# Kernel tuning notes

Measured on AMD Instinct MI355X. Metric: run time of the kernel, lower is better.

Reference implementation:

```python
import jax, jax.numpy as jnp
import numpy as np

N_NODES = 50000
N_EDGES = 1250000
IN_CH = 64
HID = 64
N_CLASSES = 10
N_GRAPHS = 128


def _xavier(key, shape):
    fan_out, fan_in = shape
    limit = np.sqrt(6.0 / (fan_in + fan_out))
    return jax.random.uniform(key, shape, jnp.float32, -limit, limit)


def setup_inputs() -> dict:
    key = jax.random.key(0)
    ks = jax.random.split(key, 12)
    x = jax.random.normal(ks[0], (N_NODES, IN_CH), jnp.float32)
    edge_index = jax.random.randint(ks[1], (2, N_EDGES), 0, N_NODES, jnp.int64)
    batch = jnp.sort(jax.random.randint(ks[2], (N_NODES,), 0, N_GRAPHS, jnp.int64))
    return {
        "x": x,
        "edge_index": edge_index,
        "batch": batch,
        # GraphConv i: lin_rel (weight+bias) applied to aggregated neighbors,
        # lin_root (no bias) applied to self features. Weights are [out, in].
        "W1_rel": _xavier(ks[3], (HID, IN_CH)), "b1": jnp.zeros((HID,), jnp.float32),
        "W1_root": _xavier(ks[4], (HID, IN_CH)),
        "W2_rel": _xavier(ks[5], (HID, HID)), "b2": jnp.zeros((HID,), jnp.float32),
        "W2_root": _xavier(ks[6], (HID, HID)),
        "W3_rel": _xavier(ks[7], (HID, HID)), "b3": jnp.zeros((HID,), jnp.float32),
        "W3_root": _xavier(ks[8], (HID, HID)),
        "W_lin": _xavier(ks[9], (N_CLASSES, HID)), "b_lin": jnp.zeros((N_CLASSES,), jnp.float32),
    }


def _graph_conv(x, src, dst, W_rel, b, W_root):
    # sum-aggregate neighbor features: gather at src, scatter-add at dst
    agg = jax.ops.segment_sum(x[src], dst, num_segments=N_NODES)  # [N, F]
    return agg @ W_rel.T + b + x @ W_root.T


def reference(x, edge_index, batch, W1_rel, b1, W1_root, W2_rel, b2, W2_root,
              W3_rel, b3, W3_root, W_lin, b_lin):
    src, dst = edge_index[0], edge_index[1]
    h = jax.nn.relu(_graph_conv(x, src, dst, W1_rel, b1, W1_root))
    h = jax.nn.relu(_graph_conv(h, src, dst, W2_rel, b2, W2_root))
    h = _graph_conv(h, src, dst, W3_rel, b3, W3_root)
    # global mean pool over graphs
    sums = jax.ops.segment_sum(h, batch, num_segments=N_GRAPHS)        # [G, HID]
    counts = jax.ops.segment_sum(jnp.ones((h.shape[0],), h.dtype), batch,
                                 num_segments=N_GRAPHS)
    pooled = sums / jnp.maximum(counts, 1.0)[:, None]
    out = pooled @ W_lin.T + b_lin  # dropout inactive in eval mode
    return (pooled, out)
```

## Files before the change

### kernel.cpp

```cpp
#include <hip/hip_runtime.h>

#define N_NODES   50000
#define HID       64
#define N_GRAPHS  128
#define N_CLASSES 10
#define NP        196
#define EPA       8192
#define PCAP      8192

typedef __attribute__((ext_vector_type(8))) short short8;
typedef __attribute__((ext_vector_type(4))) float f32x4;

__device__ __forceinline__ unsigned bf16rne(float f) {
    unsigned u = __float_as_uint(f);
    return (u + 0x7fffu + ((u >> 16) & 1u)) >> 16;
}
__device__ __forceinline__ unsigned pack_bf16x2(float lo, float hi) {
    return bf16rne(lo) | (bf16rne(hi) << 16);
}


__global__ void cvt_kernel(const float* __restrict__ x, unsigned short* __restrict__ xb,
                           int* __restrict__ gcursor) {
    if (blockIdx.x == 0 && threadIdx.x < NP) gcursor[threadIdx.x] = 0;
    int i = blockIdx.x * blockDim.x + threadIdx.x;
    if (i < N_NODES * 16) {
        float4 v = ((const float4*)x)[i];
        uint2 o;
        o.x = pack_bf16x2(v.x, v.y);
        o.y = pack_bf16x2(v.z, v.w);
        ((uint2*)xb)[i] = o;
    }
}


__global__ __launch_bounds__(256) void bucket_kernel(
    const int* __restrict__ src, const int* __restrict__ dst,
    int* __restrict__ gcursor, unsigned* __restrict__ packed, int E) {
    __shared__ int hist[NP], scp[NP], base[NP], cnt2[NP];
    __shared__ int sc[256];
    __shared__ unsigned stag[EPA];
    const int t = threadIdx.x;
    const int e0 = blockIdx.x * EPA;
    const int e1 = min(e0 + EPA, E);
    for (int i = t; i < NP; i += 256) { hist[i] = 0; cnt2[i] = 0; }
    __syncthreads();
    for (int e = e0 + t; e < e1; e += 256)
        atomicAdd(&hist[dst[e] >> 8], 1);
    __syncthreads();
    sc[t] = (t < NP) ? hist[t] : 0;
    __syncthreads();
    for (int off = 1; off < 256; off <<= 1) {
        int add = (t >= off) ? sc[t - off] : 0;
        __syncthreads();
        sc[t] += add;
        __syncthreads();
    }
    if (t < NP) {
        scp[t] = sc[t] - hist[t];
        if (hist[t] > 0) base[t] = atomicAdd(&gcursor[t], hist[t]);
    }
    __syncthreads();
    for (int e = e0 + t; e < e1; e += 256) {
        int d = dst[e], s = src[e];
        int p = d >> 8;
        int idx = scp[p] + atomicAdd(&cnt2[p], 1);
        stag[idx] = (unsigned)s | ((unsigned)(d & 255) << 16) | ((unsigned)p << 24);
    }
    __syncthreads();
    const int n = e1 - e0;
    for (int i = t; i < n; i += 256) {
        unsigned v = stag[i];
        int p = v >> 24;
        packed[(size_t)p * PCAP + base[p] + (i - scp[p])] = v & 0x00FFFFFFu;
    }
}

__global__ __launch_bounds__(256) void build_kernel(
    const unsigned* __restrict__ packed, const int* __restrict__ gcursor,
    int* __restrict__ offsets, unsigned short* __restrict__ csr) {
    __shared__ int hist[256], lofs[256], cnt[256], sc[256], gv[256];
    __shared__ unsigned short lcsr[PCAP];
    const int p = blockIdx.x, t = threadIdx.x;

    int v = (t < NP) ? gcursor[t] : 0;
    sc[t] = v; gv[t] = v;
    __syncthreads();
    for (int off = 1; off < 256; off <<= 1) {
        int add = (t >= off) ? sc[t - off] : 0;
        __syncthreads();
        sc[t] += add;
        __syncthreads();
    }
    const int pb = sc[p] - gv[p];
    const int ne = gv[p];
    if (p == NP - 1 && t == 0) offsets[N_NODES] = sc[NP - 1];
    __syncthreads();

    const unsigned* mypk = packed + (size_t)p * PCAP;
    hist[t] = 0; cnt[t] = 0;
    __syncthreads();
    for (int i = t; i < ne; i += 256)
        atomicAdd(&hist[(mypk[i] >> 16) & 255], 1);
    __syncthreads();
    sc[t] = hist[t];
    __syncthreads();
    for (int off = 1; off < 256; off <<= 1) {
        int add = (t >= off) ? sc[t - off] : 0;
        __syncthreads();
        sc[t] += add;
        __syncthreads();
    }
    lofs[t] = sc[t] - hist[t];
    int node = p * 256 + t;
    if (node < N_NODES) offsets[node] = pb + lofs[t];
    __syncthreads();
    for (int i = t; i < ne; i += 256) {
        unsigned vv = mypk[i];
        int dl = (vv >> 16) & 255;
        int slot = lofs[dl] + atomicAdd(&cnt[dl], 1);
        lcsr[slot] = (unsigned short)(vv & 0xFFFFu);
    }
    __syncthreads();
    for (int i = t; i < ne; i += 256) csr[pb + i] = lcsr[i];
}


__global__ __launch_bounds__(256) void gather_kernel(
    const unsigned short* __restrict__ hin,
    const int* __restrict__ offsets, const unsigned short* __restrict__ csr_src,
    unsigned short* __restrict__ agg) {
    const int w = threadIdx.x >> 6, lane = threadIdx.x & 63;
    const int rg = lane >> 4, c8 = lane & 15;
    const int n = blockIdx.x * 4 + w;
    const int beg = offsets[n], end = offsets[n + 1];

    float a0 = 0.f, a1 = 0.f, a2 = 0.f, a3 = 0.f;
    for (int base = beg; base < end; base += 64) {
        int cnt = min(64, end - base);
        int sidx = (base + lane < end) ? (int)csr_src[base + lane] : 0;
        for (int kb = 0; kb < cnt; kb += 32) {
            uint2 u[8];
#pragma unroll
            for (int p = 0; p < 8; ++p) {
                int e = kb + 4 * p + rg;
                int r = __shfl(sidx, e);
                u[p] = (e < cnt) ? *(const uint2*)(hin + (size_t)r * 64 + c8 * 4)
                                 : (uint2){0u, 0u};
            }
#pragma unroll
            for (int p = 0; p < 8; ++p) {
                a0 += __uint_as_float(u[p].x << 16);
                a1 += __uint_as_float(u[p].x & 0xffff0000u);
                a2 += __uint_as_float(u[p].y << 16);
                a3 += __uint_as_float(u[p].y & 0xffff0000u);
            }
        }
    }
#pragma unroll
    for (int m = 16; m <= 32; m <<= 1) {
        a0 += __shfl_xor(a0, m);
        a1 += __shfl_xor(a1, m);
        a2 += __shfl_xor(a2, m);
        a3 += __shfl_xor(a3, m);
    }
    if (rg == 0) {
        uint2 o;
        o.x = pack_bf16x2(a0, a1);
        o.y = pack_bf16x2(a2, a3);
        *(uint2*)(agg + (size_t)n * 64 + c8 * 4) = o;
    }
}


template <int RELU>
__global__ __launch_bounds__(256) void linear_kernel(
    const unsigned short* __restrict__ agg,
    const unsigned short* __restrict__ hin,
    const float* __restrict__ Wrel, const float* __restrict__ bias,
    const float* __restrict__ Wroot, unsigned short* __restrict__ hout) {
    __shared__ unsigned short outT[4][16][72];

    const int tid = threadIdx.x;
    const int w = tid >> 6, lane = tid & 63;
    const int q = lane >> 4, c = lane & 15;
    const int g0 = (blockIdx.x * 4 + w) * 16;
    if (g0 >= N_NODES) return;

    short8 brel[4][2], broot[4][2];
    float biasv[4];
#pragma unroll
    for (int t = 0; t < 4; ++t) {
        int o = t * 16 + c;
        biasv[t] = bias[o];
#pragma unroll
        for (int s = 0; s < 2; ++s) {
            const float4* pr = (const float4*)(Wrel  + o * 64 + s * 32 + q * 8);
            const float4* po = (const float4*)(Wroot + o * 64 + s * 32 + q * 8);
            float4 r0 = pr[0], r1 = pr[1], z0 = po[0], z1 = po[1];
            short8 rr, zz;
            rr[0] = (short)bf16rne(r0.x); rr[1] = (short)bf16rne(r0.y);
            rr[2] = (short)bf16rne(r0.z); rr[3] = (short)bf16rne(r0.w);
            rr[4] = (short)bf16rne(r1.x); rr[5] = (short)bf16rne(r1.y);
            rr[6] = (short)bf16rne(r1.z); rr[7] = (short)bf16rne(r1.w);
            zz[0] = (short)bf16rne(z0.x); zz[1] = (short)bf16rne(z0.y);
            zz[2] = (short)bf16rne(z0.z); zz[3] = (short)bf16rne(z0.w);
            zz[4] = (short)bf16rne(z1.x); zz[5] = (short)bf16rne(z1.y);
            zz[6] = (short)bf16rne(z1.z); zz[7] = (short)bf16rne(z1.w);
            brel[t][s] = rr; broot[t][s] = zz;
        }
    }

    const int na = min(g0 + c, N_NODES - 1);
    short8 a_agg[2], a_x[2];
#pragma unroll
    for (int s = 0; s < 2; ++s) {
        a_agg[s] = *(const short8*)(agg + (size_t)na * 64 + s * 32 + q * 8);
        a_x[s]   = *(const short8*)(hin + (size_t)na * 64 + s * 32 + q * 8);
    }

    f32x4 acc4[4];
#pragma unroll
    for (int t = 0; t < 4; ++t) {
        f32x4 a0 = {biasv[t], biasv[t], biasv[t], biasv[t]};
        a0 = __builtin_amdgcn_mfma_f32_16x16x32_bf16(a_agg[0], brel[t][0], a0, 0, 0, 0);
        a0 = __builtin_amdgcn_mfma_f32_16x16x32_bf16(a_agg[1], brel[t][1], a0, 0, 0, 0);
        a0 = __builtin_amdgcn_mfma_f32_16x16x32_bf16(a_x[0],  broot[t][0], a0, 0, 0, 0);
        a0 = __builtin_amdgcn_mfma_f32_16x16x32_bf16(a_x[1],  broot[t][1], a0, 0, 0, 0);
        acc4[t] = a0;
    }

#pragma unroll
    for (int t = 0; t < 4; ++t)
#pragma unroll
        for (int r = 0; r < 4; ++r) {
            float v = acc4[t][r];
            if (RELU) v = fmaxf(v, 0.f);
            outT[w][q * 4 + r][t * 16 + c] = (unsigned short)bf16rne(v);
        }

#pragma unroll
    for (int it = 0; it < 2; ++it) {
        int row = it * 8 + (lane >> 3);
        int ch = (lane & 7) * 8;
        int n = g0 + row;
        if (n < N_NODES) {
            short8 v = *(const short8*)&outT[w][row][ch];
            *(short8*)(hout + (size_t)n * 64 + ch) = v;
        }
    }
}


__global__ __launch_bounds__(256) void poolfinal_kernel(
    const unsigned short* __restrict__ h, const int* __restrict__ batch,
    const float* __restrict__ Wlin, const float* __restrict__ blin,
    float* __restrict__ out) {
    __shared__ float part[4][64];
    const int g = blockIdx.x;
    const int tid = threadIdx.x, w = tid >> 6, lane = tid & 63;

    int a = 0, b = N_NODES;
    while (a < b) { int m = (a + b) >> 1; if (batch[m] < g) a = m + 1; else b = m; }
    const int lo = a;
    b = N_NODES;
    while (a < b) { int m = (a + b) >> 1; if (batch[m] < g + 1) a = m + 1; else b = m; }
    const int hi = a;

    float acc = 0.f;
    for (int n = lo + w; n < hi; n += 4) {
        unsigned u = h[(size_t)n * 64 + lane];
        acc += __uint_as_float(u << 16);
    }
    part[w][lane] = acc;
    __syncthreads();
    if (w == 0) {
        float s = part[0][lane] + part[1][lane] + part[2][lane] + part[3][lane];
        float cdiv = fmaxf((float)(hi - lo), 1.0f);
        float pv = s / cdiv;
        out[g * 64 + lane] = pv;
        part[0][lane] = pv;
    }
    __syncthreads();
    if (tid < N_CLASSES) {
        float o = blin[tid];
#pragma unroll
        for (int k = 0; k < 64; ++k) o += part[0][k] * Wlin[tid * 64 + k];
        out[N_GRAPHS * 64 + g * N_CLASSES + tid] = o;
    }
}


extern "C" void kernel_launch(void* const* d_in, const int* in_sizes, int n_in,
                              void* d_out, int out_size, void* d_ws, size_t ws_size,
                              hipStream_t stream) {
    const float* x     = (const float*)d_in[0];
    const int*   ei    = (const int*)d_in[1];
    const int*   batch = (const int*)d_in[2];
    const float* W1r = (const float*)d_in[3];
    const float* b1  = (const float*)d_in[4];
    const float* W1o = (const float*)d_in[5];
    const float* W2r = (const float*)d_in[6];
    const float* b2  = (const float*)d_in[7];
    const float* W2o = (const float*)d_in[8];
    const float* W3r = (const float*)d_in[9];
    const float* b3  = (const float*)d_in[10];
    const float* W3o = (const float*)d_in[11];
    const float* Wl  = (const float*)d_in[12];
    const float* bl  = (const float*)d_in[13];
    float* out = (float*)d_out;

    const int E = in_sizes[1] / 2;
    const int* src = ei;
    const int* dst = ei + E;

    char* p = (char*)d_ws;
    unsigned short* xb  = (unsigned short*)p; p += (size_t)N_NODES * 64 * 2;
    unsigned short* h1  = (unsigned short*)p; p += (size_t)N_NODES * 64 * 2;
    unsigned short* h2  = (unsigned short*)p; p += (size_t)N_NODES * 64 * 2;
    unsigned short* agg = (unsigned short*)p; p += (size_t)N_NODES * 64 * 2;
    unsigned short* h3  = h1;
    unsigned* packed    = (unsigned*)p; p += (size_t)NP * PCAP * 4;
    unsigned short* csr = (unsigned short*)p; p += (size_t)E * 2;
    int* offsets   = (int*)p;   p += (size_t)(N_NODES + 1) * 4;
    int* gcursor   = (int*)p;   p += NP * 4;

    const int NCHUNK = (E + EPA - 1) / EPA;
    cvt_kernel<<<(N_NODES * 16 + 255) / 256, 256, 0, stream>>>(x, xb, gcursor);
    bucket_kernel<<<NCHUNK, 256, 0, stream>>>(src, dst, gcursor, packed, E);
    build_kernel<<<NP, 256, 0, stream>>>(packed, gcursor, offsets, csr);

    const int GB = N_NODES / 4;
    const int LB = (N_NODES + 63) / 64;
    gather_kernel<<<GB, 256, 0, stream>>>(xb, offsets, csr, agg);
    linear_kernel<1><<<LB, 256, 0, stream>>>(agg, xb, W1r, b1, W1o, h1);
    gather_kernel<<<GB, 256, 0, stream>>>(h1, offsets, csr, agg);
    linear_kernel<1><<<LB, 256, 0, stream>>>(agg, h1, W2r, b2, W2o, h2);
    gather_kernel<<<GB, 256, 0, stream>>>(h2, offsets, csr, agg);
    linear_kernel<0><<<LB, 256, 0, stream>>>(agg, h2, W3r, b3, W3o, h3);

    poolfinal_kernel<<<N_GRAPHS, 256, 0, stream>>>(h3, batch, Wl, bl, out);
}
```

Baseline: 281.3 us.

## Split node feature arrays into two 32-channel slabs for cache-friendly gathers

Node features, aggregates and hidden states move from a row-major [N,64] bf16 layout to two channel slabs of [N,32] each. The gather kernel now runs twice as many blocks, each summing one slab, so the working set touched at any moment is half as large and more likely to stay in L2/MALL during the random neighbor gathers. The linear, conversion and pooling kernels are updated to read and write the slab layout. The cost is that the CSR index list and offsets are read twice per layer and each gathered row segment is only 64 bytes.

```diff
diff --git a/kernel.cpp b/kernel.cpp
--- a/kernel.cpp
+++ b/kernel.cpp
@@ -7,6 +7,8 @@
 #define NP        196
 #define EPA       8192
 #define PCAP      8192
+#define NSLAB     2
+#define GBLK      12500
 
 typedef __attribute__((ext_vector_type(8))) short short8;
 typedef __attribute__((ext_vector_type(4))) float f32x4;
@@ -20,17 +22,19 @@
 }
 
 
+
 __global__ void cvt_kernel(const float* __restrict__ x, unsigned short* __restrict__ xb,
                            int* __restrict__ gcursor) {
     if (blockIdx.x == 0 && threadIdx.x < NP) gcursor[threadIdx.x] = 0;
-    int i = blockIdx.x * blockDim.x + threadIdx.x;
-    if (i < N_NODES * 16) {
-        float4 v = ((const float4*)x)[i];
-        uint2 o;
-        o.x = pack_bf16x2(v.x, v.y);
-        o.y = pack_bf16x2(v.z, v.w);
-        ((uint2*)xb)[i] = o;
-    }
+    int tid = blockIdx.x * blockDim.x + threadIdx.x;
+    if (tid >= N_NODES * 16) return;
+    int n = tid >> 4, r = tid & 15;
+    int s = r >> 3, c4 = r & 7;
+    float4 v = *(const float4*)(x + (size_t)n * 64 + r * 4);
+    uint2 o;
+    o.x = pack_bf16x2(v.x, v.y);
+    o.y = pack_bf16x2(v.z, v.w);
+    *(uint2*)(xb + ((size_t)s * N_NODES + n) * 32 + c4 * 4) = o;
 }
 
 
@@ -131,25 +135,27 @@
     const int* __restrict__ offsets, const unsigned short* __restrict__ csr_src,
     unsigned short* __restrict__ agg) {
     const int w = threadIdx.x >> 6, lane = threadIdx.x & 63;
-    const int rg = lane >> 4, c8 = lane & 15;
-    const int n = blockIdx.x * 4 + w;
+    const int s  = blockIdx.x / GBLK;
+    const int nb = blockIdx.x % GBLK;
+    const int n = nb * 4 + w;
+    const int rg = lane >> 3, cp = lane & 7;
     const int beg = offsets[n], end = offsets[n + 1];
+    const unsigned short* hs = hin + (size_t)s * N_NODES * 32;
 
     float a0 = 0.f, a1 = 0.f, a2 = 0.f, a3 = 0.f;
     for (int base = beg; base < end; base += 64) {
         int cnt = min(64, end - base);
         int sidx = (base + lane < end) ? (int)csr_src[base + lane] : 0;
         for (int kb = 0; kb < cnt; kb += 32) {
-            uint2 u[8];
-#pragma unroll
-            for (int p = 0; p < 8; ++p) {
-                int e = kb + 4 * p + rg;
+            uint2 u[4] = {{0u,0u},{0u,0u},{0u,0u},{0u,0u}};
+#pragma unroll
+            for (int p = 0; p < 4; ++p) {
+                int e = kb + p * 8 + rg;
                 int r = __shfl(sidx, e);
-                u[p] = (e < cnt) ? *(const uint2*)(hin + (size_t)r * 64 + c8 * 4)
-                                 : (uint2){0u, 0u};
+                if (e < cnt) u[p] = *(const uint2*)(hs + (size_t)r * 32 + cp * 4);
             }
 #pragma unroll
-            for (int p = 0; p < 8; ++p) {
+            for (int p = 0; p < 4; ++p) {
                 a0 += __uint_as_float(u[p].x << 16);
                 a1 += __uint_as_float(u[p].x & 0xffff0000u);
                 a2 += __uint_as_float(u[p].y << 16);
@@ -158,17 +164,17 @@
         }
     }
 #pragma unroll
-    for (int m = 16; m <= 32; m <<= 1) {
+    for (int m = 8; m <= 32; m <<= 1) {
         a0 += __shfl_xor(a0, m);
         a1 += __shfl_xor(a1, m);
         a2 += __shfl_xor(a2, m);
         a3 += __shfl_xor(a3, m);
     }
-    if (rg == 0) {
+    if (lane < 8) {
         uint2 o;
         o.x = pack_bf16x2(a0, a1);
         o.y = pack_bf16x2(a2, a3);
-        *(uint2*)(agg + (size_t)n * 64 + c8 * 4) = o;
+        *(uint2*)(agg + ((size_t)s * N_NODES + n) * 32 + lane * 4) = o;
     }
 }
 
@@ -215,8 +221,9 @@
     short8 a_agg[2], a_x[2];
 #pragma unroll
     for (int s = 0; s < 2; ++s) {
-        a_agg[s] = *(const short8*)(agg + (size_t)na * 64 + s * 32 + q * 8);
-        a_x[s]   = *(const short8*)(hin + (size_t)na * 64 + s * 32 + q * 8);
+        size_t off = ((size_t)s * N_NODES + na) * 32 + q * 8;
+        a_agg[s] = *(const short8*)(agg + off);
+        a_x[s]   = *(const short8*)(hin + off);
     }
 
     f32x4 acc4[4];
@@ -239,14 +246,13 @@
             outT[w][q * 4 + r][t * 16 + c] = (unsigned short)bf16rne(v);
         }
 
-#pragma unroll
-    for (int it = 0; it < 2; ++it) {
-        int row = it * 8 + (lane >> 3);
-        int ch = (lane & 7) * 8;
-        int n = g0 + row;
-        if (n < N_NODES) {
-            short8 v = *(const short8*)&outT[w][row][ch];
-            *(short8*)(hout + (size_t)n * 64 + ch) = v;
+    const int row = lane >> 2, c8 = (lane & 3) * 8;
+    const int n2 = g0 + row;
+#pragma unroll
+    for (int s = 0; s < 2; ++s) {
+        if (n2 < N_NODES) {
+            short8 v = *(const short8*)&outT[w][row][s * 32 + c8];
+            *(short8*)(hout + ((size_t)s * N_NODES + n2) * 32 + c8) = v;
         }
     }
 }
@@ -267,9 +273,11 @@
     while (a < b) { int m = (a + b) >> 1; if (batch[m] < g + 1) a = m + 1; else b = m; }
     const int hi = a;
 
+    const unsigned short* hs = h + (size_t)(lane >> 5) * N_NODES * 32;
+    const int c32 = lane & 31;
     float acc = 0.f;
     for (int n = lo + w; n < hi; n += 4) {
-        unsigned u = h[(size_t)n * 64 + lane];
+        unsigned u = hs[(size_t)n * 32 + c32];
         acc += __uint_as_float(u << 16);
     }
     part[w][lane] = acc;
@@ -330,7 +338,7 @@
     bucket_kernel<<<NCHUNK, 256, 0, stream>>>(src, dst, gcursor, packed, E);
     build_kernel<<<NP, 256, 0, stream>>>(packed, gcursor, offsets, csr);
 
-    const int GB = N_NODES / 4;
+    const int GB = NSLAB * GBLK;
     const int LB = (N_NODES + 63) / 64;
     gather_kernel<<<GB, 256, 0, stream>>>(xb, offsets, csr, agg);
     linear_kernel<1><<<LB, 256, 0, stream>>>(agg, xb, W1r, b1, W1o, h1);
```

New measurement: 314.3 us. 1.12x slower.
